# Optimization experiments

Measured on AMD Instinct MI355X. Metric: run time of the kernel, lower is better.

The kernel has to match this reference:

```python
import jax, jax.numpy as jnp
import numpy as np

B = 8
DIM = 256          # __init__ dim; input has 2*DIM channels
H = 32
W = 32
NUM_HEADS = 4
DH_QK = 64         # make_divisible(256*1.0, 8) // 4
DH_V = 64          # dim_out // num_heads
DQK = NUM_HEADS * DH_QK   # 256
DV = NUM_HEADS * DH_V     # 256
SCALE = DH_QK ** -0.5
HIDDEN = 4 * DIM          # mlp_ratio=4 applied to dim
DIM_OUT = DIM
EPS = 1e-5


def setup_inputs() -> dict:
    key = jax.random.key(0)
    ks = jax.random.split(key, 8)
    qkv_out = 2 * DQK + DV   # 768
    return {
        "x": jax.random.normal(ks[0], (B, 2 * DIM, H, W), jnp.float32),
        "qkv_f_w": jax.random.normal(ks[1], (qkv_out, DIM), jnp.float32) * DIM ** -0.5,
        "qkv_p_w": jax.random.normal(ks[2], (qkv_out, DIM), jnp.float32) * DIM ** -0.5,
        "height_rel": jax.random.normal(ks[3], (2 * H - 1, DH_QK), jnp.float32) * SCALE,
        "width_rel": jax.random.normal(ks[4], (2 * W - 1, DH_QK), jnp.float32) * SCALE,
        "ln_gamma": jnp.ones((2 * DV, H, W), jnp.float32),
        "ln_beta": jnp.zeros((2 * DV, H, W), jnp.float32),
        "fc1_w": jax.random.normal(ks[5], (HIDDEN, 2 * DV), jnp.float32) * (2 * DV) ** -0.5,
        "fc1_b": jnp.zeros((HIDDEN,), jnp.float32),
        "fc2_w": jax.random.normal(ks[6], (DIM_OUT, HIDDEN), jnp.float32) * HIDDEN ** -0.5,
        "fc2_b": jnp.zeros((DIM_OUT,), jnp.float32),
    }


def _rel_to_abs(x):
    # x: (b, L, 2L-1) -> (b, L, L) via the pad/reshape shift trick
    b, L, _ = x.shape
    x = jnp.pad(x, ((0, 0), (0, 0), (0, 1)))          # (b, L, 2L)
    xf = x.reshape(b, L * 2 * L)
    xf = jnp.pad(xf, ((0, 0), (0, L - 1)))
    return xf.reshape(b, L + 1, 2 * L - 1)[:, :L, L - 1:]


def _rel_logits_1d(q, rel_k, perm):
    # q: (b, h, w, d); rel_k: (2w-1, d) -> (b, h, w, h, w) after perm
    b, h, w, _ = q.shape
    x = jnp.einsum('bhwd,md->bhwm', q, rel_k).reshape(b * h, w, 2 * w - 1)
    x = _rel_to_abs(x).reshape(b, h, 1, w, w)
    x = jnp.broadcast_to(x, (b, h, h, w, w))
    return x.transpose(perm)


def _pos_embed(q, height_rel, width_rel):
    # q: (B*nh, HW, d) -> relative-position logits (B*nh, HW, HW)
    bh = q.shape[0]
    qs = q.reshape(bh, H, W, DH_QK)
    lw = _rel_logits_1d(qs, width_rel, (0, 1, 3, 2, 4))
    lh = _rel_logits_1d(qs.transpose(0, 2, 1, 3), height_rel, (0, 3, 1, 4, 2))
    return (lh + lw).reshape(bh, H * W, H * W)


def _get_qkv(x, w):
    # 1x1 conv as channel GEMM; x: (B, DIM, H, W)
    qkv = jnp.einsum('bchw,oc->bohw', x, w)
    q, k, v = jnp.split(qkv, [DQK, 2 * DQK], axis=1)
    q = q.reshape(B * NUM_HEADS, DH_QK, H * W).transpose(0, 2, 1)  # (Bh, HW, d)
    k = k.reshape(B * NUM_HEADS, DH_QK, H * W)                      # (Bh, d, HW)
    v = v.reshape(B * NUM_HEADS, DH_V, H * W).transpose(0, 2, 1)    # (Bh, HW, d)
    return q, k, v


def _apply_attn(q, k, v, height_rel, width_rel):
    logits = jnp.einsum('bnd,bdm->bnm', q, k) * SCALE + _pos_embed(q, height_rel, width_rel)
    attn = jax.nn.softmax(logits, axis=-1)
    out = jnp.einsum('bnm,bmd->bnd', attn, v)                       # (Bh, HW, dv)
    return out.transpose(0, 2, 1).reshape(B, DV, H, W)


def reference(x, qkv_f_w, qkv_p_w, height_rel, width_rel, ln_gamma, ln_beta,
              fc1_w, fc1_b, fc2_w, fc2_b):
    x1, x2 = x[:, :DIM], x[:, DIM:]
    qf, kf, vf = _get_qkv(x1, qkv_f_w)
    qp, kp, vp = _get_qkv(x2, qkv_p_w)
    out_f = _apply_attn(qf, kp, vp, height_rel, width_rel)
    out_p = _apply_attn(qp, kf, vf, height_rel, width_rel)
    xpf = jnp.concatenate([out_f, out_p], axis=1)                   # (B, 2*DV, H, W)
    # LayerNorm over normalized_shape = [2*DV, H, W]
    mean = xpf.mean(axis=(1, 2, 3), keepdims=True)
    var = jnp.var(xpf, axis=(1, 2, 3), keepdims=True)
    xpf = (xpf - mean) * jax.lax.rsqrt(var + EPS) * ln_gamma + ln_beta
    # conv-MLP (1x1 convs), exact GELU as torch default
    h = jnp.einsum('bchw,oc->bohw', xpf, fc1_w) + fc1_b[None, :, None, None]
    h = jax.nn.gelu(h, approximate=False)
    out = jnp.einsum('bchw,oc->bohw', h, fc2_w) + fc2_b[None, :, None, None]
    return out  # stride=1 -> pool is identity
```

## Files before the change

kernel.cpp:

```cpp
#include <hip/hip_runtime.h>

#define SCALE 0.125f

typedef short short8 __attribute__((ext_vector_type(8)));
typedef float f32x4 __attribute__((ext_vector_type(4)));
typedef unsigned short us8 __attribute__((ext_vector_type(8)));

__device__ __forceinline__ unsigned short f2bf(float x) {
  unsigned int u = __float_as_uint(x);
  u += 0x7fff + ((u >> 16) & 1);
  return (unsigned short)(u >> 16);
}
__device__ __forceinline__ float bf2f(unsigned short b) {
  return __uint_as_float(((unsigned int)b) << 16);
}
__device__ __forceinline__ float gelu_exact(float x) {
  return 0.5f * x * (1.0f + erff(x * 0.70710678118654752f));
}

__global__ __launch_bounds__(256)
void cast_w(const float* __restrict__ qf, const float* __restrict__ qp,
            const float* __restrict__ f1, const float* __restrict__ f2,
            unsigned short* __restrict__ wc)
{
  const int i4 = (blockIdx.x * 256 + threadIdx.x) * 4;
  const float* src; int off;
  if (i4 < 196608)      { src = qf; off = i4; }
  else if (i4 < 393216) { src = qp; off = i4 - 196608; }
  else if (i4 < 917504) { src = f1; off = i4 - 393216; }
  else                  { src = f2; off = i4 - 917504; }
  const float4 v = *(const float4*)(src + off);
  ushort4 o;
  o.x = f2bf(v.x); o.y = f2bf(v.y); o.z = f2bf(v.z); o.w = f2bf(v.w);
  *(ushort4*)(wc + i4) = o;
}

__global__ __launch_bounds__(256)
void trans_x(const float* __restrict__ x, unsigned short* __restrict__ xT)
{
  __shared__ unsigned short L[64 * 72];
  const int ch0 = blockIdx.x * 64, tok0 = blockIdx.y * 64, z = blockIdx.z;
  const int b = z & 7, path = z >> 3;
  const float* src = x + (size_t)b * 524288 + (size_t)(path * 256 + ch0) * 1024 + tok0;
#pragma unroll
  for (int t = 0; t < 4; ++t) {
    const int i = threadIdx.x + t * 256;
    const int row = i >> 4, c4 = (i & 15) * 4;
    const float4 v = *(const float4*)(src + (size_t)row * 1024 + c4);
    L[(c4 + 0) * 72 + row] = f2bf(v.x);
    L[(c4 + 1) * 72 + row] = f2bf(v.y);
    L[(c4 + 2) * 72 + row] = f2bf(v.z);
    L[(c4 + 3) * 72 + row] = f2bf(v.w);
  }
  __syncthreads();
  unsigned short* dst = xT + (size_t)z * 262144 + (size_t)tok0 * 256 + ch0;
#pragma unroll
  for (int t = 0; t < 2; ++t) {
    const int i = threadIdx.x + t * 256;
    const int row = i >> 3, c8 = (i & 7) * 8;
    *(us8*)(dst + (size_t)row * 256 + c8) = *(const us8*)&L[row * 72 + c8];
  }
}

__global__ __launch_bounds__(256)
void trans_gb(const float* __restrict__ gamma, const float* __restrict__ beta,
              unsigned short* __restrict__ gbT)
{
  __shared__ unsigned short L[64 * 72];
  const int ch0 = blockIdx.x * 64, tok0 = blockIdx.y * 64, which = blockIdx.z;
  const float* src = (which ? beta : gamma) + (size_t)ch0 * 1024 + tok0;
#pragma unroll
  for (int t = 0; t < 4; ++t) {
    const int i = threadIdx.x + t * 256;
    const int row = i >> 4, c4 = (i & 15) * 4;
    const float4 v = *(const float4*)(src + (size_t)row * 1024 + c4);
    L[(c4 + 0) * 72 + row] = f2bf(v.x);
    L[(c4 + 1) * 72 + row] = f2bf(v.y);
    L[(c4 + 2) * 72 + row] = f2bf(v.z);
    L[(c4 + 3) * 72 + row] = f2bf(v.w);
  }
  __syncthreads();
  unsigned short* dst = gbT + (size_t)which * 524288 + (size_t)tok0 * 512 + ch0;
#pragma unroll
  for (int t = 0; t < 2; ++t) {
    const int i = threadIdx.x + t * 256;
    const int row = i >> 3, c8 = (i & 7) * 8;
    *(us8*)(dst + (size_t)row * 512 + c8) = *(const us8*)&L[row * 72 + c8];
  }
}

template<int MODE, int K>
__global__ __launch_bounds__(256, 3)
void gemm_mf(const unsigned short* __restrict__ A0, const unsigned short* __restrict__ B0,
             unsigned short* __restrict__ qkT, unsigned short* __restrict__ vb,
             unsigned short* __restrict__ hT, float* __restrict__ outF,
             const float* __restrict__ bias)
{
  __shared__ unsigned short As[2][4096];
  __shared__ unsigned short Bs[2][4096];
  const int tid = threadIdx.x;
  const int lane = tid & 63, w = tid >> 6;
  const int c = lane & 15, g = lane >> 4;
  const int wm = w >> 1, wn = w & 1;
  const int m0 = blockIdx.x * 128, n0 = blockIdx.y * 128;
  const int z = blockIdx.z;

  const unsigned short* A;
  const unsigned short* B;
  if (MODE == 0) {
    A = A0 + (size_t)(z >> 3) * 196608;
    B = B0 + (size_t)z * 262144;
  } else {
    A = A0;
    B = B0 + (size_t)z * 1024 * K;
  }

  f32x4 acc[4][4];
#pragma unroll
  for (int mi = 0; mi < 4; ++mi)
#pragma unroll
    for (int ni = 0; ni < 4; ++ni) acc[mi][ni] = (f32x4){0.f, 0.f, 0.f, 0.f};

  us8 a_r[2], b_r[2];
#pragma unroll
  for (int t = 0; t < 2; ++t) {
    const int i = tid + t * 256;
    const int row = i >> 2, kc = (i & 3) * 8;
    a_r[t] = *(const us8*)(A + (size_t)(m0 + row) * K + kc);
    b_r[t] = *(const us8*)(B + (size_t)(n0 + row) * K + kc);
  }

  int buf = 0;
  const int NK = K / 32;
  for (int ks = 0; ks < NK; ++ks) {
#pragma unroll
    for (int t = 0; t < 2; ++t) {
      const int i = tid + t * 256;
      const int row = i >> 2, kc = i & 3;
      const int p = row * 32 + ((kc ^ (row & 3)) * 8);
      *(us8*)&As[buf][p] = a_r[t];
      *(us8*)&Bs[buf][p] = b_r[t];
    }
    __syncthreads();
    if (ks + 1 < NK) {
      const int k0 = (ks + 1) * 32;
#pragma unroll
      for (int t = 0; t < 2; ++t) {
        const int i = tid + t * 256;
        const int row = i >> 2, kc = (i & 3) * 8;
        a_r[t] = *(const us8*)(A + (size_t)(m0 + row) * K + k0 + kc);
        b_r[t] = *(const us8*)(B + (size_t)(n0 + row) * K + k0 + kc);
      }
    }
    short8 aF[4], bF[4];
#pragma unroll
    for (int mi = 0; mi < 4; ++mi) {
      const int row = 64 * wm + 16 * mi + c;
      aF[mi] = *(const short8*)&As[buf][row * 32 + ((g ^ (row & 3)) * 8)];
    }
#pragma unroll
    for (int ni = 0; ni < 4; ++ni) {
      const int row = 64 * wn + 16 * ni + c;
      bF[ni] = *(const short8*)&Bs[buf][row * 32 + ((g ^ (row & 3)) * 8)];
    }
#pragma unroll
    for (int mi = 0; mi < 4; ++mi)
#pragma unroll
      for (int ni = 0; ni < 4; ++ni)
        acc[mi][ni] = __builtin_amdgcn_mfma_f32_16x16x32_bf16(aF[mi], bF[ni], acc[mi][ni], 0, 0, 0);
    buf ^= 1;
  }

  if (MODE == 0) {
#pragma unroll
    for (int mi = 0; mi < 4; ++mi) {
      const int mb = m0 + 64 * wm + 16 * mi + 4 * g;
#pragma unroll
      for (int ni = 0; ni < 4; ++ni) {
        const int n = n0 + 64 * wn + 16 * ni + c;
        if (mb < 512) {
          ushort4 o4;
          o4.x = f2bf(acc[mi][ni][0]); o4.y = f2bf(acc[mi][ni][1]);
          o4.z = f2bf(acc[mi][ni][2]); o4.w = f2bf(acc[mi][ni][3]);
          *(ushort4*)(qkT + (size_t)z * 524288 + (size_t)n * 512 + mb) = o4;
        } else {
#pragma unroll
          for (int r = 0; r < 4; ++r)
            vb[(size_t)z * 262144 + (size_t)(mb - 512 + r) * 1024 + n] = f2bf(acc[mi][ni][r]);
        }
      }
    }
  } else if (MODE == 1) {
#pragma unroll
    for (int mi = 0; mi < 4; ++mi) {
      const int mb = m0 + 64 * wm + 16 * mi + 4 * g;
      const float4 b4 = *(const float4*)(bias + mb);
#pragma unroll
      for (int ni = 0; ni < 4; ++ni) {
        const int n = n0 + 64 * wn + 16 * ni + c;
        ushort4 o4;
        o4.x = f2bf(gelu_exact(acc[mi][ni][0] + b4.x));
        o4.y = f2bf(gelu_exact(acc[mi][ni][1] + b4.y));
        o4.z = f2bf(gelu_exact(acc[mi][ni][2] + b4.z));
        o4.w = f2bf(gelu_exact(acc[mi][ni][3] + b4.w));
        *(ushort4*)(hT + (size_t)z * 1048576 + (size_t)n * 1024 + mb) = o4;
      }
    }
  } else {
#pragma unroll
    for (int mi = 0; mi < 4; ++mi) {
      const int mb = m0 + 64 * wm + 16 * mi + 4 * g;
      const float4 b4 = *(const float4*)(bias + mb);
#pragma unroll
      for (int ni = 0; ni < 4; ++ni) {
        const int n = n0 + 64 * wn + 16 * ni + c;
        float* op = outF + (size_t)z * 262144 + (size_t)mb * 1024 + n;
        op[0]    = acc[mi][ni][0] + b4.x;
        op[1024] = acc[mi][ni][1] + b4.y;
        op[2048] = acc[mi][ni][2] + b4.z;
        op[3072] = acc[mi][ni][3] + b4.w;
      }
    }
  }
}

__global__ __launch_bounds__(256, 2)
void attn_k(const unsigned short* __restrict__ qkT,
            const unsigned short* __restrict__ vbuf,
            const float* __restrict__ hrel,
            const float* __restrict__ wrel,
            unsigned short* __restrict__ xpfT,
            float* __restrict__ stats)
{
  __shared__ unsigned short Kb[2][4096];
  __shared__ unsigned short Vb[2][4096];
  __shared__ unsigned short Ps[128 * 72];
  __shared__ unsigned short QHt[128 * 34];

  const int tid = threadIdx.x;
  const int lane = tid & 63, w = tid >> 6;
  const int c = lane & 15, g = lane >> 4;
  const int xb = blockIdx.x;
  const int pOut = xb >> 5, bh = xb & 31;
  const int b = bh >> 2, head = bh & 3, pKV = 1 - pOut;
  const int n0 = blockIdx.y * 128;
  const int rb = 32 * w;

  const unsigned short* Qg = qkT + (size_t)(pOut * 8 + b) * 524288 + head * 64;
  const unsigned short* Kg = qkT + (size_t)(pKV * 8 + b) * 524288 + 256 + head * 64;
  const unsigned short* Vg = vbuf + ((size_t)(pKV * 8 + b) * 256 + head * 64) * 1024;

  us8 kr[2], vr[2];
#pragma unroll
  for (int t = 0; t < 2; ++t) {
    const int i = tid + t * 256;
    const int row = i >> 3, ch = i & 7;
    kr[t] = *(const us8*)(Kg + (size_t)row * 512 + ch * 8);
    vr[t] = *(const us8*)(Vg + (size_t)row * 1024 + ch * 8);
  }

  short8 bQ[2][2];
#pragma unroll
  for (int grp = 0; grp < 2; ++grp) {
    const unsigned short* qp = Qg + (size_t)(n0 + rb + 16 * grp + c) * 512 + 8 * g;
    bQ[grp][0] = *(const short8*)(qp);
    bQ[grp][1] = *(const short8*)(qp + 32);
  }

#pragma unroll
  for (int f = 0; f < 4; ++f) {
    const int rr = 16 * f + c;
    const int rrc = rr < 63 ? rr : 62;
    const float sc = rr < 63 ? 1.f : 0.f;
    short8 w0, w1, h0, h1;
#pragma unroll
    for (int j = 0; j < 8; ++j) {
      w0[j] = f2bf(wrel[rrc * 64 + 8 * g + j] * sc);
      w1[j] = f2bf(wrel[rrc * 64 + 32 + 8 * g + j] * sc);
      h0[j] = f2bf(hrel[rrc * 64 + 8 * g + j] * sc);
      h1[j] = f2bf(hrel[rrc * 64 + 32 + 8 * g + j] * sc);
    }
#pragma unroll
    for (int grp = 0; grp < 2; ++grp) {
      f32x4 zw = {0.f, 0.f, 0.f, 0.f};
      zw = __builtin_amdgcn_mfma_f32_16x16x32_bf16(w0, bQ[grp][0], zw, 0, 0, 0);
      zw = __builtin_amdgcn_mfma_f32_16x16x32_bf16(w1, bQ[grp][1], zw, 0, 0, 0);
      f32x4 zh = {0.f, 0.f, 0.f, 0.f};
      zh = __builtin_amdgcn_mfma_f32_16x16x32_bf16(h0, bQ[grp][0], zh, 0, 0, 0);
      zh = __builtin_amdgcn_mfma_f32_16x16x32_bf16(h1, bQ[grp][1], zh, 0, 0, 0);
      const int qrow = rb + 16 * grp + c;
      ushort4 pw;
      pw.x = f2bf(zw[0]); pw.y = f2bf(zw[1]); pw.z = f2bf(zw[2]); pw.w = f2bf(zw[3]);
      *(ushort4*)&Ps[qrow * 72 + 16 * f + 4 * g] = pw;
      const int h1i = (n0 + qrow) >> 5;
#pragma unroll
      for (int r = 0; r < 4; ++r) {
        const int h2 = 16 * f + 4 * g + r - 31 + h1i;
        if (h2 >= 0 && h2 < 32) QHt[qrow * 34 + h2] = f2bf(zh[r]);
      }
    }
  }

  float qwv[2][2][4];
#pragma unroll
  for (int grp = 0; grp < 2; ++grp) {
    const int qrow = rb + 16 * grp + c;
    const int w1i = (n0 + qrow) & 31;
#pragma unroll
    for (int p = 0; p < 2; ++p)
#pragma unroll
      for (int r = 0; r < 4; ++r)
        qwv[grp][p][r] = bf2f(Ps[qrow * 72 + (16 * p + 4 * g + r - w1i + 31)]);
  }

#pragma unroll
  for (int t = 0; t < 2; ++t) {
    const int i = tid + t * 256;
    const int row = i >> 3, ch = i & 7;
    const int p = row * 64 + ((ch ^ (row & 7)) * 8);
    *(us8*)&Kb[0][p] = kr[t];
    *(us8*)&Vb[0][p] = vr[t];
  }

  float lsum[2] = {0.f, 0.f};
  f32x4 O[2][4];
#pragma unroll
  for (int grp = 0; grp < 2; ++grp)
#pragma unroll
    for (int f = 0; f < 4; ++f) O[grp][f] = (f32x4){0.f, 0.f, 0.f, 0.f};

  for (int mt = 0; mt < 16; ++mt) {
    if (mt < 15) {
      const int m0n = (mt + 1) * 64;
#pragma unroll
      for (int t = 0; t < 2; ++t) {
        const int i = tid + t * 256;
        const int row = i >> 3, ch = i & 7;
        kr[t] = *(const us8*)(Kg + (size_t)(m0n + row) * 512 + ch * 8);
        vr[t] = *(const us8*)(Vg + (size_t)row * 1024 + m0n + ch * 8);
      }
    }
    __syncthreads();
    const unsigned short* Ks = Kb[mt & 1];
    const unsigned short* Vs = Vb[mt & 1];

    short8 kA[4][2];
#pragma unroll
    for (int f = 0; f < 4; ++f) {
      const int row = 16 * f + c;
      kA[f][0] = *(const short8*)&Ks[row * 64 + ((g ^ (row & 7)) * 8)];
      kA[f][1] = *(const short8*)&Ks[row * 64 + (((4 + g) ^ (row & 7)) * 8)];
    }
#pragma unroll
    for (int grp = 0; grp < 2; ++grp) {
      const int qrow = rb + 16 * grp + c;
      const float qh0 = bf2f(QHt[qrow * 34 + 2 * mt]);
      const float qh1 = bf2f(QHt[qrow * 34 + 2 * mt + 1]);
#pragma unroll
      for (int f = 0; f < 4; ++f) {
        f32x4 z = {0.f, 0.f, 0.f, 0.f};
        z = __builtin_amdgcn_mfma_f32_16x16x32_bf16(kA[f][0], bQ[grp][0], z, 0, 0, 0);
        z = __builtin_amdgcn_mfma_f32_16x16x32_bf16(kA[f][1], bQ[grp][1], z, 0, 0, 0);
        const float qh = (f >= 2) ? qh1 : qh0;
        const float* qwp = qwv[grp][f & 1];
        const float p0 = __expf(fmaf(z[0], SCALE, qh + qwp[0]));
        const float p1 = __expf(fmaf(z[1], SCALE, qh + qwp[1]));
        const float p2 = __expf(fmaf(z[2], SCALE, qh + qwp[2]));
        const float p3 = __expf(fmaf(z[3], SCALE, qh + qwp[3]));
        lsum[grp] += (p0 + p1) + (p2 + p3);
        ushort4 pk;
        pk.x = f2bf(p0); pk.y = f2bf(p1); pk.z = f2bf(p2); pk.w = f2bf(p3);
        *(ushort4*)&Ps[qrow * 72 + 16 * f + 4 * g] = pk;
      }
    }
    short8 vB[4][2];
#pragma unroll
    for (int f = 0; f < 4; ++f) {
      const int row = 16 * f + c;
      vB[f][0] = *(const short8*)&Vs[row * 64 + ((g ^ (row & 7)) * 8)];
      vB[f][1] = *(const short8*)&Vs[row * 64 + (((4 + g) ^ (row & 7)) * 8)];
    }
#pragma unroll
    for (int grp = 0; grp < 2; ++grp) {
      const int qrow = rb + 16 * grp + c;
      const short8 aP0 = *(const short8*)&Ps[qrow * 72 + 8 * g];
      const short8 aP1 = *(const short8*)&Ps[qrow * 72 + 32 + 8 * g];
#pragma unroll
      for (int f = 0; f < 4; ++f) {
        O[grp][f] = __builtin_amdgcn_mfma_f32_16x16x32_bf16(aP0, vB[f][0], O[grp][f], 0, 0, 0);
        O[grp][f] = __builtin_amdgcn_mfma_f32_16x16x32_bf16(aP1, vB[f][1], O[grp][f], 0, 0, 0);
      }
    }
    if (mt < 15) {
#pragma unroll
      for (int t = 0; t < 2; ++t) {
        const int i = tid + t * 256;
        const int row = i >> 3, ch = i & 7;
        const int p = row * 64 + ((ch ^ (row & 7)) * 8);
        *(us8*)&Kb[(mt + 1) & 1][p] = kr[t];
        *(us8*)&Vb[(mt + 1) & 1][p] = vr[t];
      }
    }
  }

#pragma unroll
  for (int grp = 0; grp < 2; ++grp) {
    lsum[grp] += __shfl_xor(lsum[grp], 16);
    lsum[grp] += __shfl_xor(lsum[grp], 32);
  }
  float linv[2][4];
#pragma unroll
  for (int grp = 0; grp < 2; ++grp)
#pragma unroll
    for (int r = 0; r < 4; ++r)
      linv[grp][r] = 1.0f / __shfl(lsum[grp], 4 * g + r);

  float ssum = 0.f, ssq = 0.f;
#pragma unroll
  for (int grp = 0; grp < 2; ++grp)
#pragma unroll
    for (int f = 0; f < 4; ++f)
#pragma unroll
      for (int r = 0; r < 4; ++r) {
        const float v = O[grp][f][r] * linv[grp][r];
        ssum += v;
        ssq = fmaf(v, v, ssq);
        Ps[(rb + 16 * grp + 4 * g + r) * 72 + 16 * f + c] = f2bf(v);
      }
#pragma unroll
  for (int off = 1; off < 64; off <<= 1) {
    ssum += __shfl_xor(ssum, off);
    ssq  += __shfl_xor(ssq, off);
  }
  if (lane == 0) {
    atomicAdd(&stats[b * 2 + 0], ssum);
    atomicAdd(&stats[b * 2 + 1], ssq);
  }

  __syncthreads();
  unsigned short* dst = xpfT + ((size_t)b * 1024 + n0) * 512 + pOut * 256 + head * 64;
#pragma unroll
  for (int t = 0; t < 4; ++t) {
    const int i = tid + t * 256;
    const int row = i >> 3, ch = i & 7;
    *(us8*)(dst + (size_t)row * 512 + ch * 8) = *(const us8*)&Ps[row * 72 + ch * 8];
  }
}

__global__ __launch_bounds__(256)
void ln_k(const unsigned short* __restrict__ xpfT, const unsigned short* __restrict__ gbT,
          const float* __restrict__ stats, unsigned short* __restrict__ xln)
{
  const int i = blockIdx.x * 256 + threadIdx.x;
  const int b = i >> 16, off = i & 65535;
  const float invN = 1.0f / 524288.0f;
  const float mean = stats[b * 2] * invN;
  const float var = stats[b * 2 + 1] * invN - mean * mean;
  const float rstd = rsqrtf(var + 1e-5f);
  const us8 xv = *(const us8*)(xpfT + (size_t)i * 8);
  const us8 gv = *(const us8*)(gbT + (size_t)off * 8);
  const us8 bv = *(const us8*)(gbT + 524288 + (size_t)off * 8);
  us8 ov;
#pragma unroll
  for (int j = 0; j < 8; ++j)
    ov[j] = f2bf((bf2f(xv[j]) - mean) * rstd * bf2f(gv[j]) + bf2f(bv[j]));
  *(us8*)(xln + (size_t)i * 8) = ov;
}

extern "C" void kernel_launch(void* const* d_in, const int* in_sizes, int n_in,
                              void* d_out, int out_size, void* d_ws, size_t ws_size,
                              hipStream_t stream)
{
  const float* x     = (const float*)d_in[0];
  const float* qkvfw = (const float*)d_in[1];
  const float* qkvpw = (const float*)d_in[2];
  const float* hrel  = (const float*)d_in[3];
  const float* wrel  = (const float*)d_in[4];
  const float* gamma = (const float*)d_in[5];
  const float* beta  = (const float*)d_in[6];
  const float* fc1w  = (const float*)d_in[7];
  const float* fc1b  = (const float*)d_in[8];
  const float* fc2w  = (const float*)d_in[9];
  const float* fc2b  = (const float*)d_in[10];
  float* out = (float*)d_out;

  float* stats = (float*)d_ws;
  unsigned short* wc   = (unsigned short*)(stats + 64);
  unsigned short* xT   = wc + 1179648;
  unsigned short* gbT  = xT + 4194304;
  unsigned short* qkT  = gbT + 1048576;
  unsigned short* vbuf = qkT + 8388608;
  unsigned short* xpfT = vbuf + 4194304;
  unsigned short* hT   = xpfT + 4194304;

  hipMemsetAsync(stats, 0, 64 * sizeof(float), stream);

  cast_w<<<1152, 256, 0, stream>>>(qkvfw, qkvpw, fc1w, fc2w, wc);
  trans_x<<<dim3(4, 16, 16), 256, 0, stream>>>(x, xT);
  trans_gb<<<dim3(8, 16, 2), 256, 0, stream>>>(gamma, beta, gbT);

  gemm_mf<0, 256><<<dim3(6, 8, 16), 256, 0, stream>>>(
      wc, xT, qkT, vbuf, nullptr, nullptr, nullptr);

  attn_k<<<dim3(64, 8), 256, 0, stream>>>(qkT, vbuf, hrel, wrel, xpfT, stats);

  ln_k<<<2048, 256, 0, stream>>>(xpfT, gbT, stats, xT);

  gemm_mf<1, 512><<<dim3(8, 8, 8), 256, 0, stream>>>(
      wc + 393216, xT, nullptr, nullptr, hT, nullptr, fc1b);

  gemm_mf<2, 1024><<<dim3(2, 8, 8), 256, 0, stream>>>(
      wc + 917504, hT, nullptr, nullptr, nullptr, out, fc2b);
}
```

Before: 245.9 us.

## Use direct global-to-LDS loads in GEMM and split-K the fc2 GEMM with atomics

The GEMM tile loader now uses global_load_lds to write 16-byte chunks straight into shared memory. This removes the register staging and the XOR swizzle, so the LDS fragment reads are now unswizzled and may hit bank conflicts. The fc2 GEMM is split into two K halves across the z grid dimension, doubling its block count. Partial results are combined with float atomicAdd into an output that is zeroed by an extra memset, and only the first half adds the bias. The attention kernel's barrier moves to the top of the loop, before the next tile prefetch.

```diff
diff --git a/kernel.cpp b/kernel.cpp
--- a/kernel.cpp
+++ b/kernel.cpp
@@ -5,6 +5,12 @@
 typedef short short8 __attribute__((ext_vector_type(8)));
 typedef float f32x4 __attribute__((ext_vector_type(4)));
 typedef unsigned short us8 __attribute__((ext_vector_type(8)));
+
+typedef __attribute__((address_space(1))) const void gvoid;
+typedef __attribute__((address_space(3))) void svoid;
+__device__ __forceinline__ void gll16(const void* g, void* l) {
+  __builtin_amdgcn_global_load_lds((gvoid*)g, (svoid*)l, 16, 0, 0);
+}
 
 __device__ __forceinline__ unsigned short f2bf(float x) {
   unsigned int u = __float_as_uint(x);
@@ -89,7 +95,7 @@
   }
 }
 
-template<int MODE, int K>
+template<int MODE, int LD, int KLEN>
 __global__ __launch_bounds__(256, 3)
 void gemm_mf(const unsigned short* __restrict__ A0, const unsigned short* __restrict__ B0,
              unsigned short* __restrict__ qkT, unsigned short* __restrict__ vb,
@@ -107,12 +113,17 @@
 
   const unsigned short* A;
   const unsigned short* B;
+  int zb = z, kc = 0;
   if (MODE == 0) {
     A = A0 + (size_t)(z >> 3) * 196608;
     B = B0 + (size_t)z * 262144;
+  } else if (MODE == 1) {
+    A = A0;
+    B = B0 + (size_t)z * 1024 * LD;
   } else {
-    A = A0;
-    B = B0 + (size_t)z * 1024 * K;
+    zb = z >> 1; kc = z & 1;
+    A = A0 + kc * KLEN;
+    B = B0 + (size_t)zb * 1024 * LD + kc * KLEN;
   }
 
   f32x4 acc[4][4];
@@ -121,54 +132,42 @@
 #pragma unroll
     for (int ni = 0; ni < 4; ++ni) acc[mi][ni] = (f32x4){0.f, 0.f, 0.f, 0.f};
 
-  us8 a_r[2], b_r[2];
+  const int srow = tid >> 2;
+  const int skc8 = (tid & 3) * 8;
+  const int sbase = (tid & 192) * 8;
+
 #pragma unroll
   for (int t = 0; t < 2; ++t) {
-    const int i = tid + t * 256;
-    const int row = i >> 2, kc = (i & 3) * 8;
-    a_r[t] = *(const us8*)(A + (size_t)(m0 + row) * K + kc);
-    b_r[t] = *(const us8*)(B + (size_t)(n0 + row) * K + kc);
-  }
-
-  int buf = 0;
-  const int NK = K / 32;
+    gll16(A + (size_t)(m0 + srow + t * 64) * LD + skc8, &As[0][sbase + t * 2048]);
+    gll16(B + (size_t)(n0 + srow + t * 64) * LD + skc8, &Bs[0][sbase + t * 2048]);
+  }
+
+  const int NK = KLEN / 32;
   for (int ks = 0; ks < NK; ++ks) {
-#pragma unroll
-    for (int t = 0; t < 2; ++t) {
-      const int i = tid + t * 256;
-      const int row = i >> 2, kc = i & 3;
-      const int p = row * 32 + ((kc ^ (row & 3)) * 8);
-      *(us8*)&As[buf][p] = a_r[t];
-      *(us8*)&Bs[buf][p] = b_r[t];
-    }
     __syncthreads();
     if (ks + 1 < NK) {
       const int k0 = (ks + 1) * 32;
+      const int nb = (ks + 1) & 1;
 #pragma unroll
       for (int t = 0; t < 2; ++t) {
-        const int i = tid + t * 256;
-        const int row = i >> 2, kc = (i & 3) * 8;
-        a_r[t] = *(const us8*)(A + (size_t)(m0 + row) * K + k0 + kc);
-        b_r[t] = *(const us8*)(B + (size_t)(n0 + row) * K + k0 + kc);
-      }
-    }
+        gll16(A + (size_t)(m0 + srow + t * 64) * LD + k0 + skc8, &As[nb][sbase + t * 2048]);
+        gll16(B + (size_t)(n0 + srow + t * 64) * LD + k0 + skc8, &Bs[nb][sbase + t * 2048]);
+      }
+    }
+    const unsigned short* Asb = As[ks & 1];
+    const unsigned short* Bsb = Bs[ks & 1];
     short8 aF[4], bF[4];
 #pragma unroll
-    for (int mi = 0; mi < 4; ++mi) {
-      const int row = 64 * wm + 16 * mi + c;
-      aF[mi] = *(const short8*)&As[buf][row * 32 + ((g ^ (row & 3)) * 8)];
-    }
-#pragma unroll
-    for (int ni = 0; ni < 4; ++ni) {
-      const int row = 64 * wn + 16 * ni + c;
-      bF[ni] = *(const short8*)&Bs[buf][row * 32 + ((g ^ (row & 3)) * 8)];
-    }
+    for (int mi = 0; mi < 4; ++mi)
+      aF[mi] = *(const short8*)&Asb[(64 * wm + 16 * mi + c) * 32 + g * 8];
+#pragma unroll
+    for (int ni = 0; ni < 4; ++ni)
+      bF[ni] = *(const short8*)&Bsb[(64 * wn + 16 * ni + c) * 32 + g * 8];
 #pragma unroll
     for (int mi = 0; mi < 4; ++mi)
 #pragma unroll
       for (int ni = 0; ni < 4; ++ni)
         acc[mi][ni] = __builtin_amdgcn_mfma_f32_16x16x32_bf16(aF[mi], bF[ni], acc[mi][ni], 0, 0, 0);
-    buf ^= 1;
   }
 
   if (MODE == 0) {
@@ -210,15 +209,16 @@
 #pragma unroll
     for (int mi = 0; mi < 4; ++mi) {
       const int mb = m0 + 64 * wm + 16 * mi + 4 * g;
-      const float4 b4 = *(const float4*)(bias + mb);
+      float4 b4 = make_float4(0.f, 0.f, 0.f, 0.f);
+      if (kc == 0) b4 = *(const float4*)(bias + mb);
 #pragma unroll
       for (int ni = 0; ni < 4; ++ni) {
         const int n = n0 + 64 * wn + 16 * ni + c;
-        float* op = outF + (size_t)z * 262144 + (size_t)mb * 1024 + n;
-        op[0]    = acc[mi][ni][0] + b4.x;
-        op[1024] = acc[mi][ni][1] + b4.y;
-        op[2048] = acc[mi][ni][2] + b4.z;
-        op[3072] = acc[mi][ni][3] + b4.w;
+        float* op = outF + (size_t)zb * 262144 + (size_t)mb * 1024 + n;
+        atomicAdd(&op[0],    acc[mi][ni][0] + b4.x);
+        atomicAdd(&op[1024], acc[mi][ni][1] + b4.y);
+        atomicAdd(&op[2048], acc[mi][ni][2] + b4.z);
+        atomicAdd(&op[3072], acc[mi][ni][3] + b4.w);
       }
     }
   }
@@ -330,6 +330,7 @@
     for (int f = 0; f < 4; ++f) O[grp][f] = (f32x4){0.f, 0.f, 0.f, 0.f};
 
   for (int mt = 0; mt < 16; ++mt) {
+    __syncthreads();
     if (mt < 15) {
       const int m0n = (mt + 1) * 64;
 #pragma unroll
@@ -340,7 +341,6 @@
         vr[t] = *(const us8*)(Vg + (size_t)row * 1024 + m0n + ch * 8);
       }
     }
-    __syncthreads();
     const unsigned short* Ks = Kb[mt & 1];
     const unsigned short* Vs = Vb[mt & 1];
 
@@ -494,21 +494,22 @@
   unsigned short* hT   = xpfT + 4194304;
 
   hipMemsetAsync(stats, 0, 64 * sizeof(float), stream);
+  hipMemsetAsync(out, 0, (size_t)out_size * sizeof(float), stream);
 
   cast_w<<<1152, 256, 0, stream>>>(qkvfw, qkvpw, fc1w, fc2w, wc);
   trans_x<<<dim3(4, 16, 16), 256, 0, stream>>>(x, xT);
   trans_gb<<<dim3(8, 16, 2), 256, 0, stream>>>(gamma, beta, gbT);
 
-  gemm_mf<0, 256><<<dim3(6, 8, 16), 256, 0, stream>>>(
+  gemm_mf<0, 256, 256><<<dim3(6, 8, 16), 256, 0, stream>>>(
       wc, xT, qkT, vbuf, nullptr, nullptr, nullptr);
 
   attn_k<<<dim3(64, 8), 256, 0, stream>>>(qkT, vbuf, hrel, wrel, xpfT, stats);
 
   ln_k<<<2048, 256, 0, stream>>>(xpfT, gbT, stats, xT);
 
-  gemm_mf<1, 512><<<dim3(8, 8, 8), 256, 0, stream>>>(
+  gemm_mf<1, 512, 512><<<dim3(8, 8, 8), 256, 0, stream>>>(
       wc + 393216, xT, nullptr, nullptr, hT, nullptr, fc1b);
 
-  gemm_mf<2, 1024><<<dim3(2, 8, 8), 256, 0, stream>>>(
+  gemm_mf<3, 1024, 512><<<dim3(2, 8, 16), 256, 0, stream>>>(
       wc + 917504, hT, nullptr, nullptr, nullptr, out, fc2b);
 }
```

Result: no change. 249.5 us (+1.4%).
